# Optimization experiments

Hardware: AMD Instinct MI355X
Metric: run time of the kernel (lower is better)

Reference implementation:

```python
import jax, jax.numpy as jnp
import numpy as np

N = 8192
X_DIM = 256
Y_DIM = 256


def setup_inputs() -> dict:
    key = jax.random.key(0)
    kx, ky, kw = jax.random.split(key, 3)
    x_samples = jax.random.normal(kx, (N, X_DIM), dtype=jnp.float32)
    y_samples = jax.random.normal(ky, (N, Y_DIM), dtype=jnp.float32)
    # kaiming-uniform-ish init for the bilinear weight [x_dim, y_dim]
    bound = float(np.sqrt(6.0 / X_DIM))
    w = jax.random.uniform(kw, (X_DIM, Y_DIM), dtype=jnp.float32,
                           minval=-bound, maxval=bound)
    return {"x_samples": x_samples, "y_samples": y_samples, "w": w}


def reference(x_samples, y_samples, w):
    # Pairwise bilinear scores S[i, b] = x[i] @ W @ y[b]
    # (equivalent to the original's tiled einsum, without O(N^2*dim) tiles)
    n = y_samples.shape[0]
    xw = x_samples @ w                      # [N, y_dim]
    S = xw @ y_samples.T                    # [N, N], S[i, b]
    # T0[i] = S[i, i]; T1.logsumexp(dim=1)[b] = logsumexp_i S[i, b]
    t0_mean = jnp.mean(jnp.diagonal(S))
    lse_mean = jnp.mean(jax.nn.logsumexp(S, axis=0))
    lower_bound = t0_mean - (lse_mean - jnp.log(jnp.float32(n)))
    return lower_bound
```

## Files before the change

### kernel.cpp

```cpp
#include <hip/hip_runtime.h>

typedef __attribute__((ext_vector_type(8))) short bf16x8;
typedef __attribute__((ext_vector_type(4))) float f32x4;
typedef __attribute__((ext_vector_type(8))) int   i32x8;
typedef __attribute__((ext_vector_type(4))) int   i32x4;

union OpU { i32x8 v; i32x4 h[2]; };

__device__ __forceinline__ unsigned short f2bf(float f) {
    unsigned int u = __float_as_uint(f);
    u += 0x7fffu + ((u >> 16) & 1u);
    return (unsigned short)(u >> 16);
}

#define LSE_SHIFT   90.0f
#define LOG2E       1.44269504f
#define SHIFT_L2E   129.842553f

__global__ void cast_w_kernel(const float* __restrict__ w,
                              unsigned short* __restrict__ WT,
                              float* __restrict__ scal)
{
    int idx = blockIdx.x * 256 + threadIdx.x;
    const float4 wv = ((const float4*)w)[idx];
    int k = idx >> 6;
    int n0 = (idx & 63) * 4;
    WT[(size_t)(n0 + 0) * 256 + k] = f2bf(wv.x);
    WT[(size_t)(n0 + 1) * 256 + k] = f2bf(wv.y);
    WT[(size_t)(n0 + 2) * 256 + k] = f2bf(wv.z);
    WT[(size_t)(n0 + 3) * 256 + k] = f2bf(wv.w);
    if (idx == 0) {
        scal[0] = 0.f; scal[1] = 0.f;
        ((unsigned int*)scal)[2] = 0u;
    }
}

__global__ __launch_bounds__(256, 4)
void gemm0_kernel(const float* __restrict__ X, const unsigned short* __restrict__ WT,
                  const float* __restrict__ Y,
                  unsigned char* __restrict__ XWQ, unsigned char* __restrict__ YQ)
{
    __shared__ __align__(16) unsigned short As[64 * 64];
    __shared__ __align__(16) unsigned short Bs[64 * 64];

    const int tid  = threadIdx.x;
    const int lane = tid & 63;
    const int w    = tid >> 6;
    const int wm   = w >> 1, wn = w & 1;
    const int frow = lane & 15, quad = lane >> 4;
    const int rowBase = blockIdx.y * 64;
    const int colBase = blockIdx.x * 64;
    const int lb = blockIdx.y * 4 + blockIdx.x;

#pragma unroll
    for (int it = 0; it < 4; ++it) {
        int idx = lb * 1024 + it * 256 + tid;
        const float4 yv = ((const float4*)Y)[idx];
        int pk = __builtin_amdgcn_cvt_pk_fp8_f32(yv.x, yv.y, 0, 0);
        pk     = __builtin_amdgcn_cvt_pk_fp8_f32(yv.z, yv.w, pk, 1);
        ((int*)YQ)[idx] = pk;
    }

    int aOff[2][2], bOff[2][2];
#pragma unroll
    for (int mi = 0; mi < 2; ++mi)
#pragma unroll
        for (int kk = 0; kk < 2; ++kk) {
            int ka = kk * 4 + quad;
            int ra = wm * 32 + mi * 16 + frow;
            aOff[mi][kk] = ra * 64 + ((ka ^ (ra & 7)) << 3);
            int rb = wn * 32 + mi * 16 + frow;
            bOff[mi][kk] = rb * 64 + ((ka ^ (rb & 7)) << 3);
        }

    f32x4 acc[2][2];
#pragma unroll
    for (int i = 0; i < 2; ++i)
#pragma unroll
        for (int j = 0; j < 2; ++j)
            acc[i][j] = f32x4{0.f, 0.f, 0.f, 0.f};

#pragma unroll
    for (int kt = 0; kt < 4; ++kt) {
        const int k0 = kt * 64;
#pragma unroll
        for (int it = 0; it < 2; ++it) {
            int p  = it * 256 + tid;
            int r  = p >> 3;
            int s  = p & 7;
            int kc = s ^ (r & 7);
            const unsigned short* gb = WT + (size_t)(colBase + r) * 256 + k0 + (kc << 3);
            __builtin_amdgcn_global_load_lds(
                (const __attribute__((address_space(1))) void*)gb,
                (__attribute__((address_space(3))) void*)&Bs[p << 3], 16, 0, 0);
        }
#pragma unroll
        for (int it = 0; it < 4; ++it) {
            int fidx = it * 256 + tid;
            int r  = fidx >> 4;
            int c4 = fidx & 15;
            float4 v = *(const float4*)&X[(size_t)(rowBase + r) * 256 + k0 + c4 * 4];
            ushort4 u;
            u.x = f2bf(v.x); u.y = f2bf(v.y); u.z = f2bf(v.z); u.w = f2bf(v.w);
            int slot = (c4 >> 1) ^ (r & 7);
            *(ushort4*)&As[r * 64 + (slot << 3) + (c4 & 1) * 4] = u;
        }
        __syncthreads();
#pragma unroll
        for (int kk = 0; kk < 2; ++kk) {
            bf16x8 a[2], b[2];
#pragma unroll
            for (int mi = 0; mi < 2; ++mi) a[mi] = *(const bf16x8*)&As[aOff[mi][kk]];
#pragma unroll
            for (int ni = 0; ni < 2; ++ni) b[ni] = *(const bf16x8*)&Bs[bOff[ni][kk]];
#pragma unroll
            for (int mi = 0; mi < 2; ++mi)
#pragma unroll
                for (int ni = 0; ni < 2; ++ni)
                    acc[mi][ni] = __builtin_amdgcn_mfma_f32_16x16x32_bf16(
                        a[mi], b[ni], acc[mi][ni], 0, 0, 0);
        }
        __syncthreads();
    }

#pragma unroll
    for (int mi = 0; mi < 2; ++mi)
#pragma unroll
        for (int ni = 0; ni < 2; ++ni)
#pragma unroll
            for (int r2 = 0; r2 < 4; ++r2) {
                int row = rowBase + wm * 32 + mi * 16 + quad * 4 + r2;
                int col = colBase + wn * 32 + ni * 16 + frow;
                float v = acc[mi][ni][r2];
                int q = __builtin_amdgcn_cvt_pk_fp8_f32(v, v, 0, 0);
                XWQ[(size_t)row * 256 + col] = (unsigned char)(q & 0xff);
            }
}

__global__ __launch_bounds__(256, 3)
void gemm1_kernel(const unsigned char* __restrict__ A,
                  const unsigned char* __restrict__ B,
                  float* __restrict__ P, float* __restrict__ scal)
{
    __shared__ __align__(16) unsigned char As[128 * 128];
    __shared__ __align__(16) unsigned char Bs[128 * 128];
    __shared__ float lsebuf[256];

    const int tid  = threadIdx.x;
    const int lane = tid & 63;
    const int w    = tid >> 6;
    const int wm   = w >> 1, wn = w & 1;
    const int frow = lane & 15, quad = lane >> 4;
    const int rowBase = blockIdx.y * 128;
    const int colBase = blockIdx.x * 128;

    const unsigned char* gaP[4];
    const unsigned char* gbP[4];
    unsigned int ldsP[4];
#pragma unroll
    for (int it = 0; it < 4; ++it) {
        int p  = it * 256 + tid;
        int r  = p >> 3;
        int s  = p & 7;
        int kc = s ^ (r & 7);
        gaP[it] = A + (size_t)(rowBase + r) * 256 + (kc << 4);
        gbP[it] = B + (size_t)(colBase + r) * 256 + (kc << 4);
        ldsP[it] = p << 4;
    }
    const int c0 = quad * 2;
    int aAdr[4][2], bAdr[4][2];
#pragma unroll
    for (int mi = 0; mi < 4; ++mi) {
        int ra = wm * 64 + mi * 16 + frow;
        aAdr[mi][0] = ra * 128 + ((c0 ^ (ra & 7)) << 4);
        aAdr[mi][1] = ra * 128 + (((c0 + 1) ^ (ra & 7)) << 4);
        int rb = wn * 64 + mi * 16 + frow;
        bAdr[mi][0] = rb * 128 + ((c0 ^ (rb & 7)) << 4);
        bAdr[mi][1] = rb * 128 + (((c0 + 1) ^ (rb & 7)) << 4);
    }

    f32x4 acc[4][4];
#pragma unroll
    for (int i = 0; i < 4; ++i)
#pragma unroll
        for (int j = 0; j < 4; ++j)
            acc[i][j] = f32x4{0.f, 0.f, 0.f, 0.f};

#pragma unroll
    for (int it = 0; it < 4; ++it) {
        __builtin_amdgcn_global_load_lds(
            (const __attribute__((address_space(1))) void*)gaP[it],
            (__attribute__((address_space(3))) void*)&As[ldsP[it]], 16, 0, 0);
        __builtin_amdgcn_global_load_lds(
            (const __attribute__((address_space(1))) void*)gbP[it],
            (__attribute__((address_space(3))) void*)&Bs[ldsP[it]], 16, 0, 0);
    }
    __syncthreads();
    {
        i32x8 a[4], b[4];
#pragma unroll
        for (int mi = 0; mi < 4; ++mi) {
            OpU u;
            u.h[0] = *(const i32x4*)&As[aAdr[mi][0]];
            u.h[1] = *(const i32x4*)&As[aAdr[mi][1]];
            a[mi] = u.v;
        }
#pragma unroll
        for (int ni = 0; ni < 4; ++ni) {
            OpU u;
            u.h[0] = *(const i32x4*)&Bs[bAdr[ni][0]];
            u.h[1] = *(const i32x4*)&Bs[bAdr[ni][1]];
            b[ni] = u.v;
        }
#pragma unroll
        for (int mi = 0; mi < 4; ++mi)
#pragma unroll
            for (int ni = 0; ni < 4; ++ni)
                acc[mi][ni] = __builtin_amdgcn_mfma_scale_f32_16x16x128_f8f6f4(
                    a[mi], b[ni], acc[mi][ni],
                    0, 0, 0, 0x7f7f7f7f, 0, 0x7f7f7f7f);
    }
    __syncthreads();

#pragma unroll
    for (int it = 0; it < 4; ++it) {
        __builtin_amdgcn_global_load_lds(
            (const __attribute__((address_space(1))) void*)(gaP[it] + 128),
            (__attribute__((address_space(3))) void*)&As[ldsP[it]], 16, 0, 0);
        __builtin_amdgcn_global_load_lds(
            (const __attribute__((address_space(1))) void*)(gbP[it] + 128),
            (__attribute__((address_space(3))) void*)&Bs[ldsP[it]], 16, 0, 0);
    }
    __syncthreads();
    {
        i32x8 a[4], b[4];
#pragma unroll
        for (int mi = 0; mi < 4; ++mi) {
            OpU u;
            u.h[0] = *(const i32x4*)&As[aAdr[mi][0]];
            u.h[1] = *(const i32x4*)&As[aAdr[mi][1]];
            a[mi] = u.v;
        }
#pragma unroll
        for (int ni = 0; ni < 4; ++ni) {
            OpU u;
            u.h[0] = *(const i32x4*)&Bs[bAdr[ni][0]];
            u.h[1] = *(const i32x4*)&Bs[bAdr[ni][1]];
            b[ni] = u.v;
        }
#pragma unroll
        for (int mi = 0; mi < 4; ++mi)
#pragma unroll
            for (int ni = 0; ni < 4; ++ni)
                acc[mi][ni] = __builtin_amdgcn_mfma_scale_f32_16x16x128_f8f6f4(
                    a[mi], b[ni], acc[mi][ni],
                    0, 0, 0, 0x7f7f7f7f, 0, 0x7f7f7f7f);
    }

#pragma unroll
    for (int ni = 0; ni < 4; ++ni) {
        float ssum = 0.f;
#pragma unroll
        for (int mi = 0; mi < 4; ++mi)
#pragma unroll
            for (int r2 = 0; r2 < 4; ++r2)
                ssum += __builtin_amdgcn_exp2f(
                    __fmaf_rn(acc[mi][ni][r2], LOG2E, -SHIFT_L2E));
        ssum += __shfl_xor(ssum, 16);
        ssum += __shfl_xor(ssum, 32);
        if (quad == 0)
            lsebuf[wm * 128 + wn * 64 + ni * 16 + frow] = ssum;
    }
    if (blockIdx.x == blockIdx.y && wm == wn) {
        float v = 0.f;
#pragma unroll
        for (int mi = 0; mi < 4; ++mi)
#pragma unroll
            for (int r2 = 0; r2 < 4; ++r2)
                if (quad * 4 + r2 == frow) v += acc[mi][mi][r2];
#pragma unroll
        for (int o = 1; o < 64; o <<= 1) v += __shfl_xor(v, o);
        if (lane == 0) atomicAdd(&scal[0], v);
    }
    __syncthreads();
    if (tid < 128) {
        P[(size_t)blockIdx.y * 8192 + colBase + tid]
            = lsebuf[tid] + lsebuf[128 + tid];
    }
}

__global__ void combine_kernel(const float* __restrict__ P, float* __restrict__ scal,
                               float* __restrict__ out)
{
    __shared__ float red[256];
    const int tid = threadIdx.x;
    const int col = blockIdx.x * 256 + tid;
    float s = 0.f;
#pragma unroll 16
    for (int j = 0; j < 64; ++j)
        s += P[(size_t)j * 8192 + col];
    red[tid] = LSE_SHIFT + logf(s);
    __syncthreads();
#pragma unroll
    for (int o = 128; o > 0; o >>= 1) {
        if (tid < o) red[tid] += red[tid + o];
        __syncthreads();
    }
    if (tid == 0) {
        atomicAdd(&scal[1], red[0]);
        __threadfence();
        unsigned int old = __hip_atomic_fetch_add((unsigned int*)&scal[2], 1u,
                                                  __ATOMIC_ACQ_REL, __HIP_MEMORY_SCOPE_AGENT);
        if (old == 31u) {
            float t0 = __hip_atomic_load(&scal[0], __ATOMIC_RELAXED, __HIP_MEMORY_SCOPE_AGENT);
            float ls = __hip_atomic_load(&scal[1], __ATOMIC_RELAXED, __HIP_MEMORY_SCOPE_AGENT);
            const float invN = 1.f / 8192.f;
            out[0] = t0 * invN - (ls * invN - logf(8192.f));
        }
    }
}

extern "C" void kernel_launch(void* const* d_in, const int* in_sizes, int n_in,
                              void* d_out, int out_size, void* d_ws, size_t ws_size,
                              hipStream_t stream)
{
    const float* x = (const float*)d_in[0];
    const float* y = (const float*)d_in[1];
    const float* w = (const float*)d_in[2];
    float* out = (float*)d_out;

    char* ws = (char*)d_ws;
    unsigned char*  YQ  = (unsigned char*)(ws);
    unsigned char*  XWQ = (unsigned char*)(ws + 0x200000);
    unsigned short* WT  = (unsigned short*)(ws + 0x400000);
    float*          P   = (float*)        (ws + 0x420000);
    float*          scal= (float*)        (ws + 0x620000);

    cast_w_kernel<<<64, 256, 0, stream>>>(w, WT, scal);
    gemm0_kernel<<<dim3(4, 128), 256, 0, stream>>>(x, WT, y, XWQ, YQ);
    gemm1_kernel<<<dim3(64, 64), 256, 0, stream>>>(XWQ, YQ, P, scal);
    combine_kernel<<<32, 256, 0, stream>>>(P, scal, out);
}
```

Before: 105.3 us.

## Enlarge pairwise-score GEMM tile to 256x256 with 512 threads and prefetched K-halves

The fp8 score GEMM now runs with 256x256 output tiles per block, 8 waves of 512 threads, and a 1024-block grid in place of 4096 blocks. Both K halves are issued to separate LDS buffers up front, so the second half's global-to-LDS load overlaps the first half's MFMA work. A block-index swizzle is added to improve L2 locality. Larger tiles halve the redundant operand traffic and the partial-sum rows written to P (the combine loop shrinks accordingly). The cost is about 132KB of LDS per block, which limits each CU to one block and may reduce latency hiding in the exp-heavy epilogue.

```diff
diff --git a/kernel.cpp b/kernel.cpp
--- a/kernel.cpp
+++ b/kernel.cpp
@@ -137,29 +137,33 @@
             }
 }
 
-__global__ __launch_bounds__(256, 3)
+__global__ __launch_bounds__(512, 2)
 void gemm1_kernel(const unsigned char* __restrict__ A,
                   const unsigned char* __restrict__ B,
                   float* __restrict__ P, float* __restrict__ scal)
 {
-    __shared__ __align__(16) unsigned char As[128 * 128];
-    __shared__ __align__(16) unsigned char Bs[128 * 128];
-    __shared__ float lsebuf[256];
+    __shared__ __align__(16) unsigned char As[2 * 256 * 128];
+    __shared__ __align__(16) unsigned char Bs[2 * 256 * 128];
+    __shared__ float lsebuf[1024];
 
     const int tid  = threadIdx.x;
     const int lane = tid & 63;
     const int w    = tid >> 6;
-    const int wm   = w >> 1, wn = w & 1;
+    const int wm   = w >> 1;
+    const int wn   = w & 1;
     const int frow = lane & 15, quad = lane >> 4;
-    const int rowBase = blockIdx.y * 128;
-    const int colBase = blockIdx.x * 128;
+
+    const int bid = blockIdx.y * 32 + blockIdx.x;
+    const int swz = (bid & 7) * 128 + (bid >> 3);
+    const int by  = swz >> 5, bx = swz & 31;
+    const int rowBase = by * 256, colBase = bx * 256;
 
     const unsigned char* gaP[4];
     const unsigned char* gbP[4];
     unsigned int ldsP[4];
 #pragma unroll
     for (int it = 0; it < 4; ++it) {
-        int p  = it * 256 + tid;
+        int p  = it * 512 + tid;
         int r  = p >> 3;
         int s  = p & 7;
         int kc = s ^ (r & 7);
@@ -167,98 +171,74 @@
         gbP[it] = B + (size_t)(colBase + r) * 256 + (kc << 4);
         ldsP[it] = p << 4;
     }
+
     const int c0 = quad * 2;
-    int aAdr[4][2], bAdr[4][2];
+    int aAdr[4][2], bAdr[8][2];
 #pragma unroll
     for (int mi = 0; mi < 4; ++mi) {
         int ra = wm * 64 + mi * 16 + frow;
-        aAdr[mi][0] = ra * 128 + ((c0 ^ (ra & 7)) << 4);
+        aAdr[mi][0] = ra * 128 + (((c0    ) ^ (ra & 7)) << 4);
         aAdr[mi][1] = ra * 128 + (((c0 + 1) ^ (ra & 7)) << 4);
-        int rb = wn * 64 + mi * 16 + frow;
-        bAdr[mi][0] = rb * 128 + ((c0 ^ (rb & 7)) << 4);
-        bAdr[mi][1] = rb * 128 + (((c0 + 1) ^ (rb & 7)) << 4);
-    }
-
-    f32x4 acc[4][4];
+    }
+#pragma unroll
+    for (int ni = 0; ni < 8; ++ni) {
+        int rb = wn * 128 + ni * 16 + frow;
+        bAdr[ni][0] = rb * 128 + (((c0    ) ^ (rb & 7)) << 4);
+        bAdr[ni][1] = rb * 128 + (((c0 + 1) ^ (rb & 7)) << 4);
+    }
+
+    f32x4 acc[4][8];
 #pragma unroll
     for (int i = 0; i < 4; ++i)
 #pragma unroll
-        for (int j = 0; j < 4; ++j)
+        for (int j = 0; j < 8; ++j)
             acc[i][j] = f32x4{0.f, 0.f, 0.f, 0.f};
 
-#pragma unroll
-    for (int it = 0; it < 4; ++it) {
-        __builtin_amdgcn_global_load_lds(
-            (const __attribute__((address_space(1))) void*)gaP[it],
-            (__attribute__((address_space(3))) void*)&As[ldsP[it]], 16, 0, 0);
-        __builtin_amdgcn_global_load_lds(
-            (const __attribute__((address_space(1))) void*)gbP[it],
-            (__attribute__((address_space(3))) void*)&Bs[ldsP[it]], 16, 0, 0);
-    }
+#define STAGE(GOFF, LOFF)                                                     \
+    _Pragma("unroll")                                                         \
+    for (int it = 0; it < 4; ++it) {                                          \
+        __builtin_amdgcn_global_load_lds(                                     \
+            (const __attribute__((address_space(1))) void*)(gaP[it] + (GOFF)),\
+            (__attribute__((address_space(3))) void*)&As[ldsP[it] + (LOFF)],  \
+            16, 0, 0);                                                        \
+        __builtin_amdgcn_global_load_lds(                                     \
+            (const __attribute__((address_space(1))) void*)(gbP[it] + (GOFF)),\
+            (__attribute__((address_space(3))) void*)&Bs[ldsP[it] + (LOFF)],  \
+            16, 0, 0);                                                        \
+    }
+
+#define COMPUTE(LOFF)                                                         \
+    {                                                                         \
+        i32x8 a[4];                                                           \
+        _Pragma("unroll")                                                     \
+        for (int mi = 0; mi < 4; ++mi) {                                      \
+            OpU u;                                                            \
+            u.h[0] = *(const i32x4*)&As[aAdr[mi][0] + (LOFF)];                \
+            u.h[1] = *(const i32x4*)&As[aAdr[mi][1] + (LOFF)];                \
+            a[mi] = u.v;                                                      \
+        }                                                                     \
+        _Pragma("unroll")                                                     \
+        for (int ni = 0; ni < 8; ++ni) {                                      \
+            OpU ub;                                                           \
+            ub.h[0] = *(const i32x4*)&Bs[bAdr[ni][0] + (LOFF)];               \
+            ub.h[1] = *(const i32x4*)&Bs[bAdr[ni][1] + (LOFF)];               \
+            i32x8 b = ub.v;                                                   \
+            _Pragma("unroll")                                                 \
+            for (int mi = 0; mi < 4; ++mi)                                    \
+                acc[mi][ni] = __builtin_amdgcn_mfma_scale_f32_16x16x128_f8f6f4(\
+                    a[mi], b, acc[mi][ni], 0, 0, 0, 0x7f7f7f7f, 0, 0x7f7f7f7f);\
+        }                                                                     \
+    }
+
+    STAGE(0, 0);
     __syncthreads();
-    {
-        i32x8 a[4], b[4];
-#pragma unroll
-        for (int mi = 0; mi < 4; ++mi) {
-            OpU u;
-            u.h[0] = *(const i32x4*)&As[aAdr[mi][0]];
-            u.h[1] = *(const i32x4*)&As[aAdr[mi][1]];
-            a[mi] = u.v;
-        }
-#pragma unroll
-        for (int ni = 0; ni < 4; ++ni) {
-            OpU u;
-            u.h[0] = *(const i32x4*)&Bs[bAdr[ni][0]];
-            u.h[1] = *(const i32x4*)&Bs[bAdr[ni][1]];
-            b[ni] = u.v;
-        }
-#pragma unroll
-        for (int mi = 0; mi < 4; ++mi)
-#pragma unroll
-            for (int ni = 0; ni < 4; ++ni)
-                acc[mi][ni] = __builtin_amdgcn_mfma_scale_f32_16x16x128_f8f6f4(
-                    a[mi], b[ni], acc[mi][ni],
-                    0, 0, 0, 0x7f7f7f7f, 0, 0x7f7f7f7f);
-    }
+    STAGE(128, 32768);
+    COMPUTE(0);
     __syncthreads();
-
-#pragma unroll
-    for (int it = 0; it < 4; ++it) {
-        __builtin_amdgcn_global_load_lds(
-            (const __attribute__((address_space(1))) void*)(gaP[it] + 128),
-            (__attribute__((address_space(3))) void*)&As[ldsP[it]], 16, 0, 0);
-        __builtin_amdgcn_global_load_lds(
-            (const __attribute__((address_space(1))) void*)(gbP[it] + 128),
-            (__attribute__((address_space(3))) void*)&Bs[ldsP[it]], 16, 0, 0);
-    }
-    __syncthreads();
-    {
-        i32x8 a[4], b[4];
-#pragma unroll
-        for (int mi = 0; mi < 4; ++mi) {
-            OpU u;
-            u.h[0] = *(const i32x4*)&As[aAdr[mi][0]];
-            u.h[1] = *(const i32x4*)&As[aAdr[mi][1]];
-            a[mi] = u.v;
-        }
-#pragma unroll
-        for (int ni = 0; ni < 4; ++ni) {
-            OpU u;
-            u.h[0] = *(const i32x4*)&Bs[bAdr[ni][0]];
-            u.h[1] = *(const i32x4*)&Bs[bAdr[ni][1]];
-            b[ni] = u.v;
-        }
-#pragma unroll
-        for (int mi = 0; mi < 4; ++mi)
-#pragma unroll
-            for (int ni = 0; ni < 4; ++ni)
-                acc[mi][ni] = __builtin_amdgcn_mfma_scale_f32_16x16x128_f8f6f4(
-                    a[mi], b[ni], acc[mi][ni],
-                    0, 0, 0, 0x7f7f7f7f, 0, 0x7f7f7f7f);
-    }
-
-#pragma unroll
-    for (int ni = 0; ni < 4; ++ni) {
+    COMPUTE(32768);
+
+#pragma unroll
+    for (int ni = 0; ni < 8; ++ni) {
         float ssum = 0.f;
 #pragma unroll
         for (int mi = 0; mi < 4; ++mi)
@@ -269,24 +249,30 @@
         ssum += __shfl_xor(ssum, 16);
         ssum += __shfl_xor(ssum, 32);
         if (quad == 0)
-            lsebuf[wm * 128 + wn * 64 + ni * 16 + frow] = ssum;
-    }
-    if (blockIdx.x == blockIdx.y && wm == wn) {
+            lsebuf[wm * 256 + wn * 128 + ni * 16 + frow] = ssum;
+    }
+    if (bx == by && (wm >> 1) == wn) {
         float v = 0.f;
 #pragma unroll
         for (int mi = 0; mi < 4; ++mi)
 #pragma unroll
-            for (int r2 = 0; r2 < 4; ++r2)
-                if (quad * 4 + r2 == frow) v += acc[mi][mi][r2];
+            for (int ni = 0; ni < 8; ++ni)
+                if (wm * 4 + mi == wn * 8 + ni) {
+#pragma unroll
+                    for (int r2 = 0; r2 < 4; ++r2)
+                        if (quad * 4 + r2 == frow) v += acc[mi][ni][r2];
+                }
 #pragma unroll
         for (int o = 1; o < 64; o <<= 1) v += __shfl_xor(v, o);
         if (lane == 0) atomicAdd(&scal[0], v);
     }
     __syncthreads();
-    if (tid < 128) {
-        P[(size_t)blockIdx.y * 8192 + colBase + tid]
-            = lsebuf[tid] + lsebuf[128 + tid];
-    }
+    if (tid < 256) {
+        P[(size_t)by * 8192 + colBase + tid]
+            = lsebuf[tid] + lsebuf[256 + tid] + lsebuf[512 + tid] + lsebuf[768 + tid];
+    }
+#undef STAGE
+#undef COMPUTE
 }
 
 __global__ void combine_kernel(const float* __restrict__ P, float* __restrict__ scal,
@@ -297,7 +283,7 @@
     const int col = blockIdx.x * 256 + tid;
     float s = 0.f;
 #pragma unroll 16
-    for (int j = 0; j < 64; ++j)
+    for (int j = 0; j < 32; ++j)
         s += P[(size_t)j * 8192 + col];
     red[tid] = LSE_SHIFT + logf(s);
     __syncthreads();
@@ -338,6 +324,6 @@
 
     cast_w_kernel<<<64, 256, 0, stream>>>(w, WT, scal);
     gemm0_kernel<<<dim3(4, 128), 256, 0, stream>>>(x, WT, y, XWQ, YQ);
-    gemm1_kernel<<<dim3(64, 64), 256, 0, stream>>>(XWQ, YQ, P, scal);
+    gemm1_kernel<<<dim3(32, 32), 512, 0, stream>>>(XWQ, YQ, P, scal);
     combine_kernel<<<32, 256, 0, stream>>>(P, scal, out);
 }
```

New measurement: 108.0 us. 2.5% more time.

## Fuse column logsumexp combine into gemm1 via atomics and last-block election

Applied to the files above, without the earlier changes.

Removes the separate combine kernel. Each gemm1 block now atomically adds its per-column partial exp sums into a shared column accumulator, and a per-column-tile ticket counter picks the last of the 64 row blocks to take the log, reduce, and write the final scalar. This saves one kernel launch and the write and reread of the 64x8192 partial buffer. In exchange it adds 4096x128 float atomics on global memory and one ticket atomic per block.

```diff
diff --git a/kernel.cpp b/kernel.cpp
--- a/kernel.cpp
+++ b/kernel.cpp
@@ -19,6 +19,8 @@
 
 __global__ void cast_w_kernel(const float* __restrict__ w,
                               unsigned short* __restrict__ WT,
+                              float* __restrict__ PS,
+                              int* __restrict__ tick,
                               float* __restrict__ scal)
 {
     int idx = blockIdx.x * 256 + threadIdx.x;
@@ -29,6 +31,8 @@
     WT[(size_t)(n0 + 1) * 256 + k] = f2bf(wv.y);
     WT[(size_t)(n0 + 2) * 256 + k] = f2bf(wv.z);
     WT[(size_t)(n0 + 3) * 256 + k] = f2bf(wv.w);
+    if (idx < 8192) PS[idx] = 0.f;
+    if (idx < 64)   tick[idx] = 0;
     if (idx == 0) {
         scal[0] = 0.f; scal[1] = 0.f;
         ((unsigned int*)scal)[2] = 0u;
@@ -140,11 +144,13 @@
 __global__ __launch_bounds__(256, 3)
 void gemm1_kernel(const unsigned char* __restrict__ A,
                   const unsigned char* __restrict__ B,
-                  float* __restrict__ P, float* __restrict__ scal)
+                  float* __restrict__ PS, int* __restrict__ tick,
+                  float* __restrict__ scal, float* __restrict__ out)
 {
     __shared__ __align__(16) unsigned char As[128 * 128];
     __shared__ __align__(16) unsigned char Bs[128 * 128];
     __shared__ float lsebuf[256];
+    __shared__ int winflag;
 
     const int tid  = threadIdx.x;
     const int lane = tid & 63;
@@ -283,39 +289,35 @@
         if (lane == 0) atomicAdd(&scal[0], v);
     }
     __syncthreads();
-    if (tid < 128) {
-        P[(size_t)blockIdx.y * 8192 + colBase + tid]
-            = lsebuf[tid] + lsebuf[128 + tid];
-    }
-}
-
-__global__ void combine_kernel(const float* __restrict__ P, float* __restrict__ scal,
-                               float* __restrict__ out)
-{
-    __shared__ float red[256];
-    const int tid = threadIdx.x;
-    const int col = blockIdx.x * 256 + tid;
-    float s = 0.f;
-#pragma unroll 16
-    for (int j = 0; j < 64; ++j)
-        s += P[(size_t)j * 8192 + col];
-    red[tid] = LSE_SHIFT + logf(s);
-    __syncthreads();
-#pragma unroll
-    for (int o = 128; o > 0; o >>= 1) {
-        if (tid < o) red[tid] += red[tid + o];
+    if (tid < 128)
+        atomicAdd(&PS[colBase + tid], lsebuf[tid] + lsebuf[128 + tid]);
+    __syncthreads();
+
+    if (tid == 0)
+        winflag = (__hip_atomic_fetch_add(&tick[blockIdx.x], 1,
+                       __ATOMIC_ACQ_REL, __HIP_MEMORY_SCOPE_AGENT) == 63);
+    __syncthreads();
+    if (winflag) {
+        float lsum = 0.f;
+        if (tid < 128) {
+            float s = __hip_atomic_load(&PS[colBase + tid],
+                                        __ATOMIC_RELAXED, __HIP_MEMORY_SCOPE_AGENT);
+            lsum = LSE_SHIFT + logf(s);
+        }
+#pragma unroll
+        for (int o = 1; o < 64; o <<= 1) lsum += __shfl_xor(lsum, o);
+        if (lane == 0 && w < 2) lsebuf[w] = lsum;
         __syncthreads();
-    }
-    if (tid == 0) {
-        atomicAdd(&scal[1], red[0]);
-        __threadfence();
-        unsigned int old = __hip_atomic_fetch_add((unsigned int*)&scal[2], 1u,
-                                                  __ATOMIC_ACQ_REL, __HIP_MEMORY_SCOPE_AGENT);
-        if (old == 31u) {
-            float t0 = __hip_atomic_load(&scal[0], __ATOMIC_RELAXED, __HIP_MEMORY_SCOPE_AGENT);
-            float ls = __hip_atomic_load(&scal[1], __ATOMIC_RELAXED, __HIP_MEMORY_SCOPE_AGENT);
-            const float invN = 1.f / 8192.f;
-            out[0] = t0 * invN - (ls * invN - logf(8192.f));
+        if (tid == 0) {
+            atomicAdd(&scal[1], lsebuf[0] + lsebuf[1]);
+            unsigned int old = __hip_atomic_fetch_add((unsigned int*)&scal[2], 1u,
+                                  __ATOMIC_ACQ_REL, __HIP_MEMORY_SCOPE_AGENT);
+            if (old == 63u) {
+                float t0 = __hip_atomic_load(&scal[0], __ATOMIC_RELAXED, __HIP_MEMORY_SCOPE_AGENT);
+                float ls = __hip_atomic_load(&scal[1], __ATOMIC_RELAXED, __HIP_MEMORY_SCOPE_AGENT);
+                const float invN = 1.f / 8192.f;
+                out[0] = t0 * invN - (ls * invN - logf(8192.f));
+            }
         }
     }
 }
@@ -333,11 +335,11 @@
     unsigned char*  YQ  = (unsigned char*)(ws);
     unsigned char*  XWQ = (unsigned char*)(ws + 0x200000);
     unsigned short* WT  = (unsigned short*)(ws + 0x400000);
-    float*          P   = (float*)        (ws + 0x420000);
+    float*          PS  = (float*)        (ws + 0x420000);
+    int*            tick= (int*)          (ws + 0x428000);
     float*          scal= (float*)        (ws + 0x620000);
 
-    cast_w_kernel<<<64, 256, 0, stream>>>(w, WT, scal);
+    cast_w_kernel<<<64, 256, 0, stream>>>(w, WT, PS, tick, scal);
     gemm0_kernel<<<dim3(4, 128), 256, 0, stream>>>(x, WT, y, XWQ, YQ);
-    gemm1_kernel<<<dim3(64, 64), 256, 0, stream>>>(XWQ, YQ, P, scal);
-    combine_kernel<<<32, 256, 0, stream>>>(P, scal, out);
-}
+    gemm1_kernel<<<dim3(64, 64), 256, 0, stream>>>(XWQ, YQ, PS, tick, scal, out);
+}
```

New measurement: 155.7 us. 47.9% more time.
